# Kernel optimization log

Hardware: AMD Instinct MI355X
Metric: run time of the kernel (lower is better)

Reference implementation:

```python
import jax, jax.numpy as jnp
import numpy as np

H = 256
V = 10000
E = 300000


def setup_inputs() -> dict:
    key = jax.random.key(0)
    ks = jax.random.split(key, 7)
    s = 1.0 / np.sqrt(H)  # torch nn.Linear default init scale
    x = jax.random.normal(ks[0], (V, H), dtype=jnp.float32)
    e = jax.random.normal(ks[1], (E, H), dtype=jnp.float32)
    edge_index = jax.random.randint(ks[2], (2, E), 0, V, dtype=jnp.int64)
    Us_w = jax.random.uniform(ks[3], (H, H), dtype=jnp.float32, minval=-s, maxval=s)
    Us_b = jax.random.uniform(ks[4], (H,), dtype=jnp.float32, minval=-s, maxval=s)
    Vs_w = jax.random.uniform(ks[5], (H, H), dtype=jnp.float32, minval=-s, maxval=s)
    Vs_b = jax.random.uniform(ks[6], (H,), dtype=jnp.float32, minval=-s, maxval=s)
    return {"x": x, "e": e, "edge_index": edge_index,
            "Us_w": Us_w, "Us_b": Us_b, "Vs_w": Vs_w, "Vs_b": Vs_b}


def reference(x, e, edge_index, Us_w, Us_b, Vs_w, Vs_b):
    # Ue = Us(e): (E, H); Vx = Vs(x): (V, H)  [torch Linear: y = x @ W.T + b]
    Ue = jnp.einsum('eh,oh->eo', e, Us_w) + Us_b
    Vx = jnp.einsum('vh,oh->vo', x, Vs_w) + Vs_b
    src, dst = edge_index[0], edge_index[1]
    # gather + add epilogue: e_new = Ue + Vx[src] + Vx[dst]
    e_new = Ue + Vx[src] + Vx[dst]
    return e_new
```

## Files before the change

### kernel.cpp

```cpp
#include <hip/hip_runtime.h>


typedef __bf16 bf16_t;
typedef __bf16 bf16x4 __attribute__((ext_vector_type(4)));
typedef __bf16 bf16x8 __attribute__((ext_vector_type(8)));
typedef float f32x4 __attribute__((ext_vector_type(4)));
typedef float f32x8 __attribute__((ext_vector_type(8)));

#define HDIM 256
#define NV 10000
#define NE 300000

__device__ __forceinline__ void async16(const bf16_t* g, bf16_t* l) {
  __builtin_amdgcn_global_load_lds(
      (const __attribute__((address_space(1))) void*)g,
      (__attribute__((address_space(3))) void*)l, 16, 0, 0);
}

__global__ __launch_bounds__(256) void cvt_weights(
    const float* __restrict__ us, const float* __restrict__ vs,
    bf16_t* __restrict__ us_o, bf16_t* __restrict__ vs_o) {
  const int i = (blockIdx.x * 256 + threadIdx.x) * 4;
  f32x4 a = *(const f32x4*)(us + i);
  f32x4 b = *(const f32x4*)(vs + i);
  *(bf16x4*)(us_o + i) = __builtin_convertvector(a, bf16x4);
  *(bf16x4*)(vs_o + i) = __builtin_convertvector(b, bf16x4);
}

template <bool FUSED>
__global__ __launch_bounds__(256) void gemm(
    const float* __restrict__ A,
    const bf16_t* __restrict__ Wb,
    const float* __restrict__ bias,
    const int* __restrict__ sIdxG,
    const int* __restrict__ dIdxG,
    const bf16_t* __restrict__ Vx,
    float* __restrict__ outF,
    bf16_t* __restrict__ outB,
    int M) {
  __shared__ bf16_t As[128 * 32];
  __shared__ bf16_t Bs[128 * 32];
  __shared__ int sIdx[128];
  __shared__ int dIdx[128];

  const int tid = threadIdx.x;
  const int lane = tid & 63;
  const int wave = tid >> 6;
  const int wm = wave >> 1;
  const int wn = wave & 1;
  const int l15 = lane & 15;
  const int quad = lane >> 4;

  const int row0 = blockIdx.x * 128;
  const int n0 = blockIdx.y * 128;

  if (FUSED) {
    if (tid < 128) {
      int r = row0 + tid;
      if (r >= M) r = M - 1;
      sIdx[tid] = sIdxG[r];
    } else {
      int r = row0 + tid - 128;
      if (r >= M) r = M - 1;
      dIdx[tid - 128] = dIdxG[r];
    }
  }

  const int arow = tid >> 1;
  const int acol = (tid & 1) * 16;
  int garow = row0 + arow;
  if (garow >= M) garow = M - 1;
  const float* gA = A + (size_t)garow * HDIM + acol;
  bf16_t* lA = As + arow * 32 + acol;

  const bf16_t* gB0 = Wb + (size_t)(n0 + (tid >> 2)) * HDIM + (tid & 3) * 8;
  const bf16_t* gB1 = Wb + (size_t)(n0 + 64 + (tid >> 2)) * HDIM + (tid & 3) * 8;
  bf16_t* lB0 = Bs + tid * 8;
  bf16_t* lB1 = Bs + 2048 + tid * 8;

  f32x4 acc[4][4];
#pragma unroll
  for (int mi = 0; mi < 4; ++mi)
#pragma unroll
    for (int ni = 0; ni < 4; ++ni) {
      f32x4 z = {0.f, 0.f, 0.f, 0.f};
      acc[mi][ni] = z;
    }

  const int aBase = (wm * 64 + l15) * 32 + quad * 8;
  const int bBase = (wn * 64 + l15) * 32 + quad * 8;

  f32x4 pa0 = *(const f32x4*)(gA + 0);
  f32x4 pa1 = *(const f32x4*)(gA + 4);
  f32x4 pa2 = *(const f32x4*)(gA + 8);
  f32x4 pa3 = *(const f32x4*)(gA + 12);

  for (int k0 = 0; k0 < HDIM; k0 += 32) {
    async16(gB0 + k0, lB0);
    async16(gB1 + k0, lB1);

    f32x4 c0 = pa0, c1 = pa1, c2 = pa2, c3 = pa3;
    if (k0 + 32 < HDIM) {
      pa0 = *(const f32x4*)(gA + k0 + 32);
      pa1 = *(const f32x4*)(gA + k0 + 36);
      pa2 = *(const f32x4*)(gA + k0 + 40);
      pa3 = *(const f32x4*)(gA + k0 + 44);
    }
    f32x8 lo = {c0[0], c0[1], c0[2], c0[3], c1[0], c1[1], c1[2], c1[3]};
    f32x8 hi = {c2[0], c2[1], c2[2], c2[3], c3[0], c3[1], c3[2], c3[3]};
    *(bf16x8*)(lA + 0) = __builtin_convertvector(lo, bf16x8);
    *(bf16x8*)(lA + 8) = __builtin_convertvector(hi, bf16x8);

    __syncthreads();

    bf16x8 af[4], bfr[4];
#pragma unroll
    for (int mi = 0; mi < 4; ++mi)
      af[mi] = *(const bf16x8*)(As + aBase + mi * 16 * 32);
#pragma unroll
    for (int ni = 0; ni < 4; ++ni)
      bfr[ni] = *(const bf16x8*)(Bs + bBase + ni * 16 * 32);
#pragma unroll
    for (int mi = 0; mi < 4; ++mi)
#pragma unroll
      for (int ni = 0; ni < 4; ++ni)
        acc[mi][ni] = __builtin_amdgcn_mfma_f32_16x16x32_bf16(
            af[mi], bfr[ni], acc[mi][ni], 0, 0, 0);
    __syncthreads();
  }

  float bcol[4];
#pragma unroll
  for (int ni = 0; ni < 4; ++ni)
    bcol[ni] = bias[n0 + wn * 64 + ni * 16 + l15];

#pragma unroll
  for (int mi = 0; mi < 4; ++mi) {
#pragma unroll
    for (int r = 0; r < 4; ++r) {
      const int rl = wm * 64 + mi * 16 + quad * 4 + r;
      const int row = row0 + rl;
      if (row < M) {
        const bf16_t* vs = nullptr;
        const bf16_t* vd = nullptr;
        if (FUSED) {
          vs = Vx + (size_t)sIdx[rl] * HDIM;
          vd = Vx + (size_t)dIdx[rl] * HDIM;
        }
#pragma unroll
        for (int ni = 0; ni < 4; ++ni) {
          const int col = n0 + wn * 64 + ni * 16 + l15;
          float v = acc[mi][ni][r] + bcol[ni];
          if (FUSED) {
            v += (float)vs[col] + (float)vd[col];
            outF[(size_t)row * HDIM + col] = v;
          } else {
            outB[(size_t)row * HDIM + col] = (bf16_t)v;
          }
        }
      }
    }
  }
}

extern "C" void kernel_launch(void* const* d_in, const int* in_sizes, int n_in,
                              void* d_out, int out_size, void* d_ws,
                              size_t ws_size, hipStream_t stream) {
  const float* x = (const float*)d_in[0];
  const float* e = (const float*)d_in[1];
  const int* edge = (const int*)d_in[2];
  const float* Us_w = (const float*)d_in[3];
  const float* Us_b = (const float*)d_in[4];
  const float* Vs_w = (const float*)d_in[5];
  const float* Vs_b = (const float*)d_in[6];
  float* out = (float*)d_out;

  bf16_t* us_w_b = (bf16_t*)d_ws;
  bf16_t* vs_w_b = (bf16_t*)((char*)d_ws + (128 << 10));
  bf16_t* Vx = (bf16_t*)((char*)d_ws + (256 << 10));

  dim3 blk(256, 1, 1);

  cvt_weights<<<dim3(64, 1, 1), blk, 0, stream>>>(Us_w, Vs_w, us_w_b, vs_w_b);

  dim3 g1((NV + 127) / 128, 2, 1);
  gemm<false><<<g1, blk, 0, stream>>>(x, vs_w_b, Vs_b, nullptr, nullptr,
                                      nullptr, nullptr, Vx, NV);

  dim3 g2((NE + 127) / 128, 2, 1);
  gemm<true><<<g2, blk, 0, stream>>>(e, us_w_b, Us_b, edge, edge + NE, Vx, out,
                                     nullptr, NE);
}
```

Measured before the change: 635.9 us.

## Load GEMM operands directly to registers, drop LDS and use full-N tiles

```diff
diff --git a/kernel.cpp b/kernel.cpp
--- a/kernel.cpp
+++ b/kernel.cpp
@@ -10,12 +10,6 @@
 #define HDIM 256
 #define NV 10000
 #define NE 300000
-
-__device__ __forceinline__ void async16(const bf16_t* g, bf16_t* l) {
-  __builtin_amdgcn_global_load_lds(
-      (const __attribute__((address_space(1))) void*)g,
-      (__attribute__((address_space(3))) void*)l, 16, 0, 0);
-}
 
 __global__ __launch_bounds__(256) void cvt_weights(
     const float* __restrict__ us, const float* __restrict__ vs,
@@ -38,45 +32,25 @@
     float* __restrict__ outF,
     bf16_t* __restrict__ outB,
     int M) {
-  __shared__ bf16_t As[128 * 32];
-  __shared__ bf16_t Bs[128 * 32];
-  __shared__ int sIdx[128];
-  __shared__ int dIdx[128];
-
   const int tid = threadIdx.x;
   const int lane = tid & 63;
-  const int wave = tid >> 6;
-  const int wm = wave >> 1;
-  const int wn = wave & 1;
+  const int wn = tid >> 6;
   const int l15 = lane & 15;
   const int quad = lane >> 4;
 
-  const int row0 = blockIdx.x * 128;
-  const int n0 = blockIdx.y * 128;
+  const int row0 = blockIdx.x * 64;
 
-  if (FUSED) {
-    if (tid < 128) {
-      int r = row0 + tid;
-      if (r >= M) r = M - 1;
-      sIdx[tid] = sIdxG[r];
-    } else {
-      int r = row0 + tid - 128;
-      if (r >= M) r = M - 1;
-      dIdx[tid - 128] = dIdxG[r];
-    }
+  const float* gA[4];
+#pragma unroll
+  for (int mi = 0; mi < 4; ++mi) {
+    int r = row0 + mi * 16 + l15;
+    if (r >= M) r = M - 1;
+    gA[mi] = A + (size_t)r * HDIM + quad * 8;
   }
-
-  const int arow = tid >> 1;
-  const int acol = (tid & 1) * 16;
-  int garow = row0 + arow;
-  if (garow >= M) garow = M - 1;
-  const float* gA = A + (size_t)garow * HDIM + acol;
-  bf16_t* lA = As + arow * 32 + acol;
-
-  const bf16_t* gB0 = Wb + (size_t)(n0 + (tid >> 2)) * HDIM + (tid & 3) * 8;
-  const bf16_t* gB1 = Wb + (size_t)(n0 + 64 + (tid >> 2)) * HDIM + (tid & 3) * 8;
-  bf16_t* lB0 = Bs + tid * 8;
-  bf16_t* lB1 = Bs + 2048 + tid * 8;
+  const bf16_t* gB[4];
+#pragma unroll
+  for (int ni = 0; ni < 4; ++ni)
+    gB[ni] = Wb + (size_t)(wn * 64 + ni * 16 + l15) * HDIM + quad * 8;
 
   f32x4 acc[4][4];
 #pragma unroll
@@ -87,76 +61,69 @@
       acc[mi][ni] = z;
     }
 
-  const int aBase = (wm * 64 + l15) * 32 + quad * 8;
-  const int bBase = (wn * 64 + l15) * 32 + quad * 8;
-
-  f32x4 pa0 = *(const f32x4*)(gA + 0);
-  f32x4 pa1 = *(const f32x4*)(gA + 4);
-  f32x4 pa2 = *(const f32x4*)(gA + 8);
-  f32x4 pa3 = *(const f32x4*)(gA + 12);
+  f32x4 pa0[4], pa1[4];
+#pragma unroll
+  for (int mi = 0; mi < 4; ++mi) {
+    pa0[mi] = *(const f32x4*)(gA[mi] + 0);
+    pa1[mi] = *(const f32x4*)(gA[mi] + 4);
+  }
 
   for (int k0 = 0; k0 < HDIM; k0 += 32) {
-    async16(gB0 + k0, lB0);
-    async16(gB1 + k0, lB1);
-
-    f32x4 c0 = pa0, c1 = pa1, c2 = pa2, c3 = pa3;
-    if (k0 + 32 < HDIM) {
-      pa0 = *(const f32x4*)(gA + k0 + 32);
-      pa1 = *(const f32x4*)(gA + k0 + 36);
-      pa2 = *(const f32x4*)(gA + k0 + 40);
-      pa3 = *(const f32x4*)(gA + k0 + 44);
-    }
-    f32x8 lo = {c0[0], c0[1], c0[2], c0[3], c1[0], c1[1], c1[2], c1[3]};
-    f32x8 hi = {c2[0], c2[1], c2[2], c2[3], c3[0], c3[1], c3[2], c3[3]};
-    *(bf16x8*)(lA + 0) = __builtin_convertvector(lo, bf16x8);
-    *(bf16x8*)(lA + 8) = __builtin_convertvector(hi, bf16x8);
-
-    __syncthreads();
-
-    bf16x8 af[4], bfr[4];
-#pragma unroll
-    for (int mi = 0; mi < 4; ++mi)
-      af[mi] = *(const bf16x8*)(As + aBase + mi * 16 * 32);
+    bf16x8 bfr[4];
 #pragma unroll
     for (int ni = 0; ni < 4; ++ni)
-      bfr[ni] = *(const bf16x8*)(Bs + bBase + ni * 16 * 32);
+      bfr[ni] = *(const bf16x8*)(gB[ni] + k0);
+
+    bf16x8 af[4];
+#pragma unroll
+    for (int mi = 0; mi < 4; ++mi) {
+      f32x4 c0 = pa0[mi], c1 = pa1[mi];
+      f32x8 t = {c0[0], c0[1], c0[2], c0[3], c1[0], c1[1], c1[2], c1[3]};
+      af[mi] = __builtin_convertvector(t, bf16x8);
+    }
+
+    if (k0 + 32 < HDIM) {
+#pragma unroll
+      for (int mi = 0; mi < 4; ++mi) {
+        pa0[mi] = *(const f32x4*)(gA[mi] + k0 + 32);
+        pa1[mi] = *(const f32x4*)(gA[mi] + k0 + 36);
+      }
+    }
+
 #pragma unroll
     for (int mi = 0; mi < 4; ++mi)
 #pragma unroll
       for (int ni = 0; ni < 4; ++ni)
         acc[mi][ni] = __builtin_amdgcn_mfma_f32_16x16x32_bf16(
             af[mi], bfr[ni], acc[mi][ni], 0, 0, 0);
-    __syncthreads();
   }
 
   float bcol[4];
 #pragma unroll
   for (int ni = 0; ni < 4; ++ni)
-    bcol[ni] = bias[n0 + wn * 64 + ni * 16 + l15];
+    bcol[ni] = bias[wn * 64 + ni * 16 + l15];
 
 #pragma unroll
   for (int mi = 0; mi < 4; ++mi) {
 #pragma unroll
     for (int r = 0; r < 4; ++r) {
-      const int rl = wm * 64 + mi * 16 + quad * 4 + r;
-      const int row = row0 + rl;
+      const int row = row0 + mi * 16 + quad * 4 + r;
       if (row < M) {
-        const bf16_t* vs = nullptr;
-        const bf16_t* vd = nullptr;
         if (FUSED) {
-          vs = Vx + (size_t)sIdx[rl] * HDIM;
-          vd = Vx + (size_t)dIdx[rl] * HDIM;
-        }
+          const int si = sIdxG[row];
+          const int di = dIdxG[row];
+          const bf16_t* vs = Vx + (size_t)si * HDIM + wn * 64 + l15;
+          const bf16_t* vd = Vx + (size_t)di * HDIM + wn * 64 + l15;
+          float* orow = outF + (size_t)row * HDIM + wn * 64 + l15;
 #pragma unroll
-        for (int ni = 0; ni < 4; ++ni) {
-          const int col = n0 + wn * 64 + ni * 16 + l15;
-          float v = acc[mi][ni][r] + bcol[ni];
-          if (FUSED) {
-            v += (float)vs[col] + (float)vd[col];
-            outF[(size_t)row * HDIM + col] = v;
-          } else {
-            outB[(size_t)row * HDIM + col] = (bf16_t)v;
-          }
+          for (int ni = 0; ni < 4; ++ni)
+            orow[ni * 16] = acc[mi][ni][r] + bcol[ni] +
+                            (float)vs[ni * 16] + (float)vd[ni * 16];
+        } else {
+          bf16_t* orow = outB + (size_t)row * HDIM + wn * 64 + l15;
+#pragma unroll
+          for (int ni = 0; ni < 4; ++ni)
+            orow[ni * 16] = (bf16_t)(acc[mi][ni][r] + bcol[ni]);
         }
       }
     }
@@ -183,11 +150,11 @@
 
   cvt_weights<<<dim3(64, 1, 1), blk, 0, stream>>>(Us_w, Vs_w, us_w_b, vs_w_b);
 
-  dim3 g1((NV + 127) / 128, 2, 1);
+  dim3 g1((NV + 63) / 64, 1, 1);
   gemm<false><<<g1, blk, 0, stream>>>(x, vs_w_b, Vs_b, nullptr, nullptr,
                                       nullptr, nullptr, Vx, NV);
 
-  dim3 g2((NE + 127) / 128, 2, 1);
+  dim3 g2((NE + 63) / 64, 1, 1);
   gemm<true><<<g2, blk, 0, stream>>>(e, us_w_b, Us_b, edge, edge + NE, Vx, out,
                                      nullptr, NE);
 }
```

New measurement: 721.0 us. 13.4% more time.
